# Optimization experiments

Hardware: AMD Instinct MI355X
Metric: run time of the kernel (lower is better)

## Reference

```python
import jax, jax.numpy as jnp
import numpy as np

NEG_INF = -1e10  # masked_fill value from the torch module


def setup_inputs() -> dict:
    key = jax.random.key(0)
    k1, k2, k3, k4, k5 = jax.random.split(key, 5)
    B, S, H = 64, 2048, 512
    return {
        "decoder_hidden": jax.random.normal(k1, (B, H), dtype=jnp.float32),
        "encoder_outputs": jax.random.normal(k2, (B, S, 2 * H), dtype=jnp.float32),
        "mask": jnp.ones((B, S), dtype=jnp.int32),
        "Wd": jax.random.normal(k3, (H, H), dtype=jnp.float32) * (1.0 / np.sqrt(H)),
        "We": jax.random.normal(k4, (2 * H, H), dtype=jnp.float32) * (1.0 / np.sqrt(2 * H)),
        "v": jax.random.normal(k5, (H,), dtype=jnp.float32) * (1.0 / np.sqrt(H)),
    }


def reference(decoder_hidden, encoder_outputs, mask, Wd, We, v):
    # decoder_proj: (B, H); encoder_proj: (B, S, H)
    dec_proj = decoder_hidden @ Wd
    enc_proj = jnp.einsum("bse,eh->bsh", encoder_outputs, We)
    energy = jnp.tanh(dec_proj[:, None, :] + enc_proj)  # (B, S, H)
    scores = jnp.einsum("bsh,h->bs", energy, v)  # (B, S)
    scores = jnp.where(mask == 0, NEG_INF, scores)
    attn_weights = jax.nn.softmax(scores, axis=1)  # (B, S)
    context = jnp.einsum("bs,bsd->bd", attn_weights, encoder_outputs)  # (B, 2H)
    return (context, attn_weights)
```

## Files before the change

kernel.cpp:

```cpp
#include <hip/hip_runtime.h>

typedef _Float16 f16;
typedef f16  f16x4 __attribute__((ext_vector_type(4)));
typedef f16  f16x8 __attribute__((ext_vector_type(8)));
typedef float f32x4 __attribute__((ext_vector_type(4)));

#define B_  64
#define S_  2048
#define H_  512
#define K_  1024

__device__ __forceinline__ float fast_tanh(float x){
  float ax = fabsf(x);
  float t  = __expf(-2.0f*ax);
  float r  = (1.0f - t) / (1.0f + t);
  return x < 0.0f ? -r : r;
}

__global__ __launch_bounds__(256) void prep_k(const float* __restrict__ We,
                                              f16* __restrict__ Bg,
                                              const float* __restrict__ dh,
                                              const float* __restrict__ Wd,
                                              float* __restrict__ dp,
                                              const float* __restrict__ vvg,
                                              float* __restrict__ vC){
  __shared__ float s_dh[512];
  if (blockIdx.x < 2048){
    int idx = blockIdx.x*256 + threadIdx.x;
    int k = idx >> 9, col = idx & 511;
    Bg[((k>>3)<<12) + (col<<3) + (k&7)] = (f16)We[idx];
  } else if (blockIdx.x < 2176){
    int idx = blockIdx.x - 2048;
    int b = idx >> 1, cg = idx & 1;
    int col = (cg<<8) + threadIdx.x;
    for (int i = threadIdx.x; i < 512; i += 256) s_dh[i] = dh[(b<<9) + i];
    __syncthreads();
    float a0=0.f,a1=0.f,a2=0.f,a3=0.f;
    for (int k = 0; k < 512; k += 4){
      a0 += s_dh[k+0]*Wd[(k+0)*512 + col];
      a1 += s_dh[k+1]*Wd[(k+1)*512 + col];
      a2 += s_dh[k+2]*Wd[(k+2)*512 + col];
      a3 += s_dh[k+3]*Wd[(k+3)*512 + col];
    }
    dp[(b<<9) + col] = (a0+a1)+(a2+a3);
  } else {
    int t = threadIdx.x;
    float a = fabsf(vvg[t]) + fabsf(vvg[t+256]);
    #pragma unroll
    for (int o = 32; o >= 1; o >>= 1) a += __shfl_xor(a, o);
    if ((t & 63) == 0) s_dh[t>>6] = a;
    __syncthreads();
    if (t == 0) vC[0] = s_dh[0]+s_dh[1]+s_dh[2]+s_dh[3];
  }
}

__global__ __launch_bounds__(512, 2) void fused_k(
    const float* __restrict__ enc,
    const f16*   __restrict__ Bg,
    const float* __restrict__ dp,
    const float* __restrict__ vvg,
    const float* __restrict__ vC,
    const int*   __restrict__ mask,
    float*       __restrict__ pbuf,
    float*       __restrict__ denom,
    float*       __restrict__ part)
{
  __shared__ __align__(16) f16 At[2][2048];
  __shared__ __align__(16) f16 Bt[2][16384];
  __shared__ float s_sc[64];

  const int tid  = threadIdx.x;
  const int lane = tid & 63;
  const int wave = tid >> 6;
  const int b    = blockIdx.x >> 5;
  const int s0   = (blockIdx.x & 31) << 6;

  if (tid < 64) s_sc[tid] = 0.0f;

  const int arow = tid >> 3;
  const int akq  = tid & 7;
  const float* aG = enc + ((size_t)(b*S_ + s0 + arow) << 10) + (akq << 2);
  const int aDst = ((akq>>1)<<9) + (arow<<3) + ((akq&1)<<2);

  const int r16 = lane & 15, g = lane >> 4;
  const int aFrag = (g<<9)  + (r16<<3);
  const int colb  = wave << 6;
  const int bFrag = (g<<12) + ((colb + r16)<<3);

  f32x4 acc[4][4] = {};

  auto stage = [&](int buf, int t){
    const f16* src = Bg + ((size_t)t << 14);
    #pragma unroll
    for (int i = 0; i < 4; ++i){
      int slot = (i<<9) + tid;
      __builtin_amdgcn_global_load_lds(
          (const __attribute__((address_space(1))) void*)(src + (slot<<3)),
          (__attribute__((address_space(3))) void*)(&Bt[buf][slot<<3]),
          16, 0, 0);
    }
    f32x4 a4 = *(const f32x4*)(aG + (t<<5));
    f16x4 h4; h4[0]=(f16)a4[0]; h4[1]=(f16)a4[1]; h4[2]=(f16)a4[2]; h4[3]=(f16)a4[3];
    *(f16x4*)&At[buf][aDst] = h4;
  };

  stage(0, 0);
  __syncthreads();

  for (int t = 0; t < 32; ++t){
    const int cur = t & 1;
    if (t < 31) stage(cur^1, t+1);
    f16x8 bfr[4];
    #pragma unroll
    for (int n = 0; n < 4; ++n) bfr[n] = *(const f16x8*)&Bt[cur][bFrag + (n<<7)];
    #pragma unroll
    for (int m = 0; m < 4; ++m){
      f16x8 af = *(const f16x8*)&At[cur][aFrag + (m<<7)];
      #pragma unroll
      for (int n = 0; n < 4; ++n)
        acc[m][n] = __builtin_amdgcn_mfma_f32_16x16x32_f16(af, bfr[n], acc[m][n], 0, 0, 0);
    }
    __syncthreads();
  }

  float dpv[4], vvv[4];
  #pragma unroll
  for (int n = 0; n < 4; ++n){
    int c = colb + (n<<4) + r16;
    dpv[n] = dp[(b<<9) + c];
    vvv[n] = vvg[c];
  }
  float sp[4][4] = {};
  #pragma unroll
  for (int m = 0; m < 4; ++m)
    #pragma unroll
    for (int n = 0; n < 4; ++n)
      #pragma unroll
      for (int r = 0; r < 4; ++r){
        float e = fast_tanh(acc[m][n][r] + dpv[n]);
        sp[m][r] += vvv[n]*e;
      }
  #pragma unroll
  for (int m = 0; m < 4; ++m)
    #pragma unroll
    for (int r = 0; r < 4; ++r){
      float x = sp[m][r];
      x += __shfl_xor(x, 1);
      x += __shfl_xor(x, 2);
      x += __shfl_xor(x, 4);
      x += __shfl_xor(x, 8);
      if (r16 == 0) atomicAdd(&s_sc[(m<<4) + (g<<2) + r], x);
    }
  __syncthreads();

  const float C = vC[0];
  if (tid < 64){
    float s = s_sc[tid];
    int mk = mask[(b<<11) + s0 + tid];
    float p = mk ? __expf(s - C) : 0.0f;
    s_sc[tid] = p;
    pbuf[(b<<11) + s0 + tid] = p;
    float d = p;
    #pragma unroll
    for (int o = 32; o >= 1; o >>= 1) d += __shfl_xor(d, o);
    if (tid == 0) denom[(b<<5) + (blockIdx.x & 31)] = d;
  }
  __syncthreads();

  {
    const float2* e2 = (const float2*)(enc + ((size_t)(b*S_ + s0) << 10)) + tid;
    float ax = 0.f, ay = 0.f;
    #pragma unroll 4
    for (int s = 0; s < 64; ++s){
      float w = s_sc[s];
      float2 x = e2[s*512];
      ax += w * x.x; ay += w * x.y;
    }
    float2* pp = (float2*)part + ((size_t)blockIdx.x << 9) + tid;
    *pp = make_float2(ax, ay);
  }
}

__global__ __launch_bounds__(256) void combine_k(const float* __restrict__ part,
                                                 const float* __restrict__ denom,
                                                 const float* __restrict__ pbuf,
                                                 float* __restrict__ ctx,
                                                 float* __restrict__ attn){
  const int b = blockIdx.x, tid = threadIdx.x;
  float D = 0.f;
  #pragma unroll
  for (int c = 0; c < 32; ++c) D += denom[(b<<5) + c];
  D = fmaxf(D, 1e-37f);
  const float inv = 1.0f / D;

  f32x4 acc = {0.f,0.f,0.f,0.f};
  const f32x4* p4 = (const f32x4*)part;
  #pragma unroll
  for (int c = 0; c < 32; ++c)
    acc += p4[(((b<<5)+c)<<8) + tid];
  ((f32x4*)ctx)[(b<<8) + tid] = acc * inv;

  #pragma unroll
  for (int i = 0; i < 8; ++i){
    int s = tid + (i<<8);
    attn[(b<<11) + s] = pbuf[(b<<11) + s] * inv;
  }
}

extern "C" void kernel_launch(void* const* d_in, const int* in_sizes, int n_in,
                              void* d_out, int out_size, void* d_ws, size_t ws_size,
                              hipStream_t stream){
  (void)in_sizes; (void)n_in; (void)out_size;
  const size_t WS_NEED = 1712384u + 8388608u;
  if (ws_size < WS_NEED) return;

  const float* dec_h = (const float*)d_in[0];
  const float* enc   = (const float*)d_in[1];
  const int*   mask  = (const int*)d_in[2];
  const float* Wd    = (const float*)d_in[3];
  const float* We    = (const float*)d_in[4];
  const float* v     = (const float*)d_in[5];
  float* out  = (float*)d_out;
  float* ctx  = out;
  float* attn = out + B_*2*H_;

  char* ws = (char*)d_ws;
  f16*   Bg     = (f16*)ws;
  float* dproj  = (float*)(ws + 1048576);
  float* vC     = (float*)(ws + 1179648);
  float* pbuf   = (float*)(ws + 1179904);
  float* denom  = (float*)(ws + 1704192);
  float* part   = (float*)(ws + 1712384);

  prep_k   <<<2177, 256, 0, stream>>>(We, Bg, dec_h, Wd, dproj, v, vC);
  fused_k  <<<2048, 512, 0, stream>>>(enc, Bg, dproj, v, vC, mask, pbuf, denom, part);
  combine_k<<<B_, 256, 0, stream>>>(part, denom, pbuf, ctx, attn);
}
```

Before: 296.8 us.

## Prefetch A tiles two stages ahead in registers and swizzle A LDS layout

The GEMM main loop now loads the fp32 encoder tile for iteration t+2 into registers while the B tile for t+1 is copied into LDS asynchronously. It replaces __syncthreads with manual s_waitcnt vmcnt(1) plus s_barrier, so the outstanding A load can stay in flight across the barrier. The A tile's LDS layout is also XOR-swizzled on the row index to reduce bank conflicts when MFMA fragments are read. This costs extra registers and depends on a hand-counted vmcnt, which is fragile if the compiler orders or merges loads differently.

```diff
diff --git a/kernel.cpp b/kernel.cpp
--- a/kernel.cpp
+++ b/kernel.cpp
@@ -79,17 +79,18 @@
 
   const int arow = tid >> 3;
   const int akq  = tid & 7;
+  const int kgrp = akq >> 1, apar = akq & 1;
   const float* aG = enc + ((size_t)(b*S_ + s0 + arow) << 10) + (akq << 2);
-  const int aDst = ((akq>>1)<<9) + (arow<<3) + ((akq&1)<<2);
+  const int aDst = (kgrp<<9) + ((arow ^ (kgrp<<1))<<3) + (apar<<2);
 
   const int r16 = lane & 15, g = lane >> 4;
-  const int aFrag = (g<<9)  + (r16<<3);
+  const int aFrag = (g<<9) + ((r16 ^ (g<<1))<<3);
   const int colb  = wave << 6;
   const int bFrag = (g<<12) + ((colb + r16)<<3);
 
   f32x4 acc[4][4] = {};
 
-  auto stage = [&](int buf, int t){
+  auto stageB = [&](int buf, int t){
     const f16* src = Bg + ((size_t)t << 14);
     #pragma unroll
     for (int i = 0; i < 4; ++i){
@@ -99,17 +100,37 @@
           (__attribute__((address_space(3))) void*)(&Bt[buf][slot<<3]),
           16, 0, 0);
     }
-    f32x4 a4 = *(const f32x4*)(aG + (t<<5));
+  };
+  auto loadA = [&](int t)->f32x4 { return *(const f32x4*)(aG + (t<<5)); };
+  auto putA  = [&](f32x4 a4, int buf){
     f16x4 h4; h4[0]=(f16)a4[0]; h4[1]=(f16)a4[1]; h4[2]=(f16)a4[2]; h4[3]=(f16)a4[3];
     *(f16x4*)&At[buf][aDst] = h4;
   };
 
-  stage(0, 0);
-  __syncthreads();
+  f32x4 aCur = {}, aNext = {};
+  {
+    f32x4 a0 = loadA(0);
+    __builtin_amdgcn_sched_barrier(0);
+    stageB(0, 0);
+    __builtin_amdgcn_sched_barrier(0);
+    aCur = loadA(1);
+    __builtin_amdgcn_sched_barrier(0);
+    putA(a0, 0);
+  }
+  asm volatile("s_waitcnt vmcnt(1) lgkmcnt(0)" ::: "memory");
+  __builtin_amdgcn_sched_barrier(0);
+  __builtin_amdgcn_s_barrier();
+  __builtin_amdgcn_sched_barrier(0);
 
   for (int t = 0; t < 32; ++t){
     const int cur = t & 1;
-    if (t < 31) stage(cur^1, t+1);
+    if (t < 31){
+      stageB(cur^1, t+1);
+      __builtin_amdgcn_sched_barrier(0);
+      aNext = loadA(t+2 < 32 ? t+2 : 31);
+      __builtin_amdgcn_sched_barrier(0);
+      putA(aCur, cur^1);
+    }
     f16x8 bfr[4];
     #pragma unroll
     for (int n = 0; n < 4; ++n) bfr[n] = *(const f16x8*)&Bt[cur][bFrag + (n<<7)];
@@ -120,7 +141,11 @@
       for (int n = 0; n < 4; ++n)
         acc[m][n] = __builtin_amdgcn_mfma_f32_16x16x32_f16(af, bfr[n], acc[m][n], 0, 0, 0);
     }
-    __syncthreads();
+    asm volatile("s_waitcnt vmcnt(1) lgkmcnt(0)" ::: "memory");
+    __builtin_amdgcn_sched_barrier(0);
+    __builtin_amdgcn_s_barrier();
+    __builtin_amdgcn_sched_barrier(0);
+    aCur = aNext;
   }
 
   float dpv[4], vvv[4];
```

New measurement: 296.5 us. About the same (-0.1%).

## Halve fused kernel threads, widen per-wave tile, single-buffer B with register-prefetched A

Applied to the files above, without the earlier changes.

Cuts the fused block from 512 to 256 threads. Each wave now computes a 64x128 output tile (4x8 MFMA accumulators), which raises B-fragment reuse per A load. The B tile in LDS drops from double to single buffering to free LDS for three blocks per CU. A is prefetched into registers two steps ahead and stored as XOR-swizzled f16x8 to avoid bank conflicts, and the context pass now uses float4 loads. The trade-off is that single-buffered B needs two barriers per k-step with the B load exposed, and the larger accumulator set increases register pressure.

```diff
diff --git a/kernel.cpp b/kernel.cpp
--- a/kernel.cpp
+++ b/kernel.cpp
@@ -54,7 +54,7 @@
   }
 }
 
-__global__ __launch_bounds__(512, 2) void fused_k(
+__global__ __launch_bounds__(256, 3) void fused_k(
     const float* __restrict__ enc,
     const f16*   __restrict__ Bg,
     const float* __restrict__ dp,
@@ -66,7 +66,7 @@
     float*       __restrict__ part)
 {
   __shared__ __align__(16) f16 At[2][2048];
-  __shared__ __align__(16) f16 Bt[2][16384];
+  __shared__ __align__(16) f16 Bt[16384];
   __shared__ float s_sc[64];
 
   const int tid  = threadIdx.x;
@@ -77,69 +77,89 @@
 
   if (tid < 64) s_sc[tid] = 0.0f;
 
-  const int arow = tid >> 3;
-  const int akq  = tid & 7;
-  const float* aG = enc + ((size_t)(b*S_ + s0 + arow) << 10) + (akq << 2);
-  const int aDst = ((akq>>1)<<9) + (arow<<3) + ((akq&1)<<2);
+  const int arow = tid >> 2;
+  const int ag   = tid & 3;
+  const float* aG = enc + ((size_t)(b*S_ + s0 + arow) << 10) + (ag << 3);
+  const int aDst = (ag << 9) + ((arow ^ (ag << 2)) << 3);
 
   const int r16 = lane & 15, g = lane >> 4;
-  const int aFrag = (g<<9)  + (r16<<3);
-  const int colb  = wave << 6;
-  const int bFrag = (g<<12) + ((colb + r16)<<3);
-
-  f32x4 acc[4][4] = {};
-
-  auto stage = [&](int buf, int t){
+  const int colb = wave << 7;
+
+  f32x4 acc[4][8] = {};
+
+  auto stageB = [&](int t){
     const f16* src = Bg + ((size_t)t << 14);
     #pragma unroll
-    for (int i = 0; i < 4; ++i){
-      int slot = (i<<9) + tid;
+    for (int i = 0; i < 8; ++i){
+      int slot = (i << 8) + tid;
       __builtin_amdgcn_global_load_lds(
           (const __attribute__((address_space(1))) void*)(src + (slot<<3)),
-          (__attribute__((address_space(3))) void*)(&Bt[buf][slot<<3]),
+          (__attribute__((address_space(3))) void*)(&Bt[slot<<3]),
           16, 0, 0);
     }
-    f32x4 a4 = *(const f32x4*)(aG + (t<<5));
-    f16x4 h4; h4[0]=(f16)a4[0]; h4[1]=(f16)a4[1]; h4[2]=(f16)a4[2]; h4[3]=(f16)a4[3];
-    *(f16x4*)&At[buf][aDst] = h4;
   };
-
-  stage(0, 0);
-  __syncthreads();
+  struct A8 { f32x4 lo, hi; };
+  auto loadA = [&](int t)->A8 {
+    const float* p = aG + (t<<5);
+    A8 r; r.lo = *(const f32x4*)p; r.hi = *(const f32x4*)(p+4); return r;
+  };
+  auto putA = [&](A8 a, int buf){
+    f16x8 h;
+    h[0]=(f16)a.lo[0]; h[1]=(f16)a.lo[1]; h[2]=(f16)a.lo[2]; h[3]=(f16)a.lo[3];
+    h[4]=(f16)a.hi[0]; h[5]=(f16)a.hi[1]; h[6]=(f16)a.hi[2]; h[7]=(f16)a.hi[3];
+    *(f16x8*)&At[buf][aDst] = h;
+  };
+
+  stageB(0);
+  A8 aR = loadA(0);
+  putA(aR, 0);
+  __syncthreads();
+  aR = loadA(1);
 
   for (int t = 0; t < 32; ++t){
     const int cur = t & 1;
-    if (t < 31) stage(cur^1, t+1);
-    f16x8 bfr[4];
-    #pragma unroll
-    for (int n = 0; n < 4; ++n) bfr[n] = *(const f16x8*)&Bt[cur][bFrag + (n<<7)];
-    #pragma unroll
-    for (int m = 0; m < 4; ++m){
-      f16x8 af = *(const f16x8*)&At[cur][aFrag + (m<<7)];
+    f16x8 af[4];
+    #pragma unroll
+    for (int m = 0; m < 4; ++m)
+      af[m] = *(const f16x8*)&At[cur][(g<<9) + ((((m<<4)+r16) ^ (g<<2))<<3)];
+    #pragma unroll
+    for (int n = 0; n < 8; ++n){
+      f16x8 bfr = *(const f16x8*)&Bt[(g<<12) + ((colb + (n<<4) + r16)<<3)];
       #pragma unroll
-      for (int n = 0; n < 4; ++n)
-        acc[m][n] = __builtin_amdgcn_mfma_f32_16x16x32_f16(af, bfr[n], acc[m][n], 0, 0, 0);
-    }
-    __syncthreads();
-  }
-
-  float dpv[4], vvv[4];
-  #pragma unroll
-  for (int n = 0; n < 4; ++n){
+      for (int m = 0; m < 4; ++m)
+        acc[m][n] = __builtin_amdgcn_mfma_f32_16x16x32_f16(af[m], bfr, acc[m][n], 0, 0, 0);
+    }
+    if (t < 31){
+      putA(aR, cur^1);
+      __syncthreads();
+      stageB(t+1);
+      __syncthreads();
+      aR = loadA(t+2 <= 31 ? t+2 : 31);
+    }
+  }
+
+  float dpv[8], vvv[8];
+  #pragma unroll
+  for (int n = 0; n < 8; ++n){
     int c = colb + (n<<4) + r16;
     dpv[n] = dp[(b<<9) + c];
     vvv[n] = vvg[c];
   }
-  float sp[4][4] = {};
+  float sp[4][4];
   #pragma unroll
   for (int m = 0; m < 4; ++m)
     #pragma unroll
-    for (int n = 0; n < 4; ++n)
+    for (int r = 0; r < 4; ++r) sp[m][r] = 0.f;
+  #pragma unroll
+  for (int m = 0; m < 4; ++m)
+    #pragma unroll
+    for (int n = 0; n < 8; ++n)
       #pragma unroll
       for (int r = 0; r < 4; ++r){
         float e = fast_tanh(acc[m][n][r] + dpv[n]);
         sp[m][r] += vvv[n]*e;
       }
+  __syncthreads();
   #pragma unroll
   for (int m = 0; m < 4; ++m)
     #pragma unroll
@@ -168,16 +188,15 @@
   __syncthreads();
 
   {
-    const float2* e2 = (const float2*)(enc + ((size_t)(b*S_ + s0) << 10)) + tid;
-    float ax = 0.f, ay = 0.f;
+    const f32x4* e4 = (const f32x4*)(enc + ((size_t)(b*S_ + s0) << 10)) + tid;
+    f32x4 acc4 = {0.f,0.f,0.f,0.f};
     #pragma unroll 4
     for (int s = 0; s < 64; ++s){
       float w = s_sc[s];
-      float2 x = e2[s*512];
-      ax += w * x.x; ay += w * x.y;
-    }
-    float2* pp = (float2*)part + ((size_t)blockIdx.x << 9) + tid;
-    *pp = make_float2(ax, ay);
+      f32x4 x = e4[s*256];
+      acc4 += w * x;
+    }
+    ((f32x4*)part)[(blockIdx.x<<8) + tid] = acc4;
   }
 }
 
@@ -233,6 +252,6 @@
   float* part   = (float*)(ws + 1712384);
 
   prep_k   <<<2177, 256, 0, stream>>>(We, Bg, dec_h, Wd, dproj, v, vC);
-  fused_k  <<<2048, 512, 0, stream>>>(enc, Bg, dproj, v, vC, mask, pbuf, denom, part);
+  fused_k  <<<2048, 256, 0, stream>>>(enc, Bg, dproj, v, vC, mask, pbuf, denom, part);
   combine_k<<<B_, 256, 0, stream>>>(part, denom, pbuf, ctx, attn);
 }
```

New measurement: 333.9 us. 1.12x slower.
